# Kernel optimization log

Measured on AMD Instinct MI355X. Metric: run time of the kernel, lower is better.

Reference implementation:

```python
import jax, jax.numpy as jnp
import numpy as np

NG = 64  # number of graphs in the batch (global_add_pool output rows)

def _bn(x, g, b):
    # BatchNorm1d, training-mode batch statistics over dim 0
    mu = x.mean(0)
    var = x.var(0)
    return (x - mu) * jax.lax.rsqrt(var + 1e-5) * g + b

def _ln(x, g, b):
    mu = x.mean(-1, keepdims=True)
    var = x.var(-1, keepdims=True)
    return (x - mu) * jax.lax.rsqrt(var + 1e-5) * g + b

def _gine(x, ei, ea, eps, w1, b1, w2, b2, n):
    # GINEConv: mlp((1+eps)*x + sum_dst ReLU(x[src] + ea))
    msg = jax.nn.relu(x[ei[0]] + ea)
    agg = jax.ops.segment_sum(msg, ei[1], num_segments=n)
    h = (1.0 + eps) * x + agg
    return jax.nn.relu(h @ w1 + b1) @ w2 + b2

def setup_inputs() -> dict:
    key = jax.random.key(0)
    H, L, RW = 128, 4, 16
    Nn, m, kk = 4096, 2, 32
    S = Nn * m; SK = S * kk
    Ei, Eg = 1048576, 65536
    Vatom, Vbond = 128, 16
    ks = jax.random.split(key, 24)
    f = lambda i, shape: jax.random.normal(ks[i], shape, jnp.float32) * 0.02
    # intra edges sampled within each subgraph block to honor locality
    subs = jax.random.randint(ks[11], (Ei,), 0, S)
    src = subs * kk + jax.random.randint(ks[12], (Ei,), 0, kk)
    dst = subs * kk + jax.random.randint(ks[13], (Ei,), 0, kk)
    inp = {
        "atom_emb": f(0, (Vatom, H)), "bond_emb": f(1, (Vbond, H)),
        "rwse_w": f(2, (RW, H)), "rwse_b": jnp.zeros((H,), jnp.float32),
        "rwse": jax.random.uniform(ks[3], (Nn, RW), jnp.float32),
        "l_eps": jnp.zeros((L,), jnp.float32),
        "l_w1": f(4, (L, H, H)), "l_b1": jnp.zeros((L, H), jnp.float32),
        "l_w2": f(5, (L, H, H)), "l_b2": jnp.zeros((L, H), jnp.float32),
        "l_bng": jnp.ones((L, H), jnp.float32), "l_bnb": jnp.zeros((L, H), jnp.float32),
        "g_eps": jnp.zeros((L,), jnp.float32),
        "g_w1": f(6, (L, H, H)), "g_b1": jnp.zeros((L, H), jnp.float32),
        "g_w2": f(7, (L, H, H)), "g_b2": jnp.zeros((L, H), jnp.float32),
        "g_bng": jnp.ones((L, H), jnp.float32), "g_bnb": jnp.zeros((L, H), jnp.float32),
        "bcast_w": f(8, (L, H, H)),
        "cat_w1": f(9, (L, 2 * H, H)), "cat_b1": jnp.zeros((L, H), jnp.float32),
        "cat_w2": f(10, (L, H, H)), "cat_b2": jnp.zeros((L, H), jnp.float32),
        "ln_g": jnp.ones((L, H), jnp.float32), "ln_b": jnp.zeros((L, H), jnp.float32),
        "x_ids": jax.random.randint(ks[14], (SK,), 0, Vatom),
        "intra_ei": jnp.stack([src, dst]),
        "intra_ea_ids": jax.random.randint(ks[15], (Ei,), 0, Vbond),
        "global_ei": jax.random.randint(ks[16], (2, Eg), 0, Nn),
        "global_ea_ids": jax.random.randint(ks[17], (Eg,), 0, Vbond),
        "node_ids": jax.random.randint(ks[18], (SK,), 0, Nn),
        "valid": jax.random.randint(ks[19], (SK,), 0, 2),
        "batch": jnp.sort(jax.random.randint(ks[20], (Nn,), 0, NG)),
        "k": 32,
    }
    return inp

def reference(atom_emb, bond_emb, rwse_w, rwse_b, rwse, l_eps, l_w1, l_b1, l_w2, l_b2, l_bng, l_bnb, g_eps, g_w1, g_b1, g_w2, g_b2, g_bng, g_bnb, bcast_w, cat_w1, cat_b1, cat_w2, cat_b2, ln_g, ln_b, x_ids, intra_ei, intra_ea_ids, global_ei, global_ea_ids, node_ids, valid, batch, k):
    SK = x_ids.shape[0]; Nn = rwse.shape[0]
    S = SK // k; m = S // Nn
    H = atom_emb.shape[1]; L = l_eps.shape[0]
    ea_flat = bond_emb[intra_ea_ids]          # [Ei, H]
    g_ea = bond_emb[global_ea_ids]            # [Eg, H]
    valid_f = valid.astype(jnp.float32)[:, None]
    h = (atom_emb[x_ids] + jax.nn.relu(rwse @ rwse_w + rwse_b)[node_ids]) * valid_f  # [SK, H]
    node_assign = jnp.repeat(jnp.arange(Nn), m)   # [S]
    root_idx = jnp.arange(S) * k                  # subgraph roots in flat layout
    for i in range(L):
        h_in = h
        h_local = _bn(jax.nn.relu(_gine(h, intra_ei, ea_flat, l_eps[i], l_w1[i], l_b1[i], l_w2[i], l_b2[i], SK)), l_bng[i], l_bnb[i])
        # scatter-mean of root reps onto original nodes (each node has exactly m subgraphs)
        h_node = jax.ops.segment_sum(h[root_idx], node_assign, num_segments=Nn) / m
        h_cross = _bn(jax.nn.relu(_gine(h_node, global_ei, g_ea, g_eps[i], g_w1[i], g_b1[i], g_w2[i], g_b2[i], Nn)), g_bng[i], g_bnb[i])
        h_node = h_node + h_cross
        # broadcast projected node reps back to every flat subgraph position
        h_b = jnp.repeat((h_node @ bcast_w[i])[node_assign], k, axis=0)  # [SK, H]
        h_cat = jnp.concatenate([h_local, h_b], axis=-1)
        h_new = _ln(jax.nn.gelu(h_cat @ cat_w1[i] + cat_b1[i], approximate=False) @ cat_w2[i] + cat_b2[i], ln_g[i], ln_b[i])
        h = (h_in + h_new) * valid_f
    # per-subgraph masked mean (h is already zero at invalid rows)
    cnt = valid_f.reshape(S, k, 1).sum(1)
    h_sub = h.reshape(S, k, H).sum(1) / jnp.maximum(cnt, 1.0)   # [S, H]
    h_nodef = h_sub.reshape(Nn, m, H).mean(1)                   # [Nn, H]
    return jax.ops.segment_sum(h_nodef, batch, num_segments=NG) # [NG, H]
```

## Files before the change

kernel.cpp:

```cpp
#include <hip/hip_runtime.h>
#include <hip/hip_bf16.h>

#define H 128
#define HH 16384
#define LNUM 4
#define NN 4096
#define SS 8192
#define SKK 262144
#define EI 1048576
#define EG 65536
#define NGRAPH 64

typedef unsigned short u16;
typedef unsigned int u32;
typedef __attribute__((ext_vector_type(8))) short s16x8;
typedef __attribute__((ext_vector_type(4))) float f32x4;

__device__ __forceinline__ float b2f(u32 u){ return __uint_as_float(u<<16); }
__device__ __forceinline__ u16 f2b(float f){
  union { __hip_bfloat16 b; u16 u; } x;
  x.b=__float2bfloat16(f);
  return x.u;
}
__device__ __forceinline__ void unp8(uint4 v, float* f){
  f[0]=b2f(v.x&0xFFFF); f[1]=b2f(v.x>>16);
  f[2]=b2f(v.y&0xFFFF); f[3]=b2f(v.y>>16);
  f[4]=b2f(v.z&0xFFFF); f[5]=b2f(v.z>>16);
  f[6]=b2f(v.w&0xFFFF); f[7]=b2f(v.w>>16);
}
__device__ __forceinline__ void unp4(uint2 v, float* f){
  f[0]=b2f(v.x&0xFFFF); f[1]=b2f(v.x>>16);
  f[2]=b2f(v.y&0xFFFF); f[3]=b2f(v.y>>16);
}
__device__ __forceinline__ uint4 pk8(const float* f){
  uint4 r;
  r.x=(u32)f2b(f[0])|((u32)f2b(f[1])<<16);
  r.y=(u32)f2b(f[2])|((u32)f2b(f[3])<<16);
  r.z=(u32)f2b(f[4])|((u32)f2b(f[5])<<16);
  r.w=(u32)f2b(f[6])|((u32)f2b(f[7])<<16);
  return r;
}
__device__ __forceinline__ uint2 pk4(const float* f){
  uint2 r;
  r.x=(u32)f2b(f[0])|((u32)f2b(f[1])<<16);
  r.y=(u32)f2b(f[2])|((u32)f2b(f[3])<<16);
  return r;
}

struct CvtArgs {
  const void* p[26];
  int start[27];
};
struct TransArgs { int src[28]; };

__global__ void k_sniff(const u16* __restrict__ a, int* __restrict__ flag){
  __shared__ int cnt;
  if(threadIdx.x==0) cnt=0;
  __syncthreads();
  int big=0;
  for(int i=threadIdx.x;i<2048;i+=256){
    int e=(a[i]>>7)&0xFF;
    if(e>=127) big++;
  }
  atomicAdd(&cnt,big);
  __syncthreads();
  if(threadIdx.x==0) *flag=(cnt<16)?1:0;
}

__global__ void k_convert(CvtArgs args, const int* __restrict__ flag, float* __restrict__ dst){
  int fl=*flag;
  int total=args.start[26];
  for(int i=blockIdx.x*blockDim.x+threadIdx.x;i<total;i+=gridDim.x*blockDim.x){
    int a=0;
    while(args.start[a+1]<=i) a++;
    int j=i-args.start[a];
    float v;
    if(fl) v=b2f(((const u16*)args.p[a])[j]);
    else   v=((const float*)args.p[a])[j];
    dst[i]=v;
  }
}

__global__ __launch_bounds__(256) void k_trans(const float* __restrict__ par, TransArgs ta, u16* __restrict__ wt){
  const float* s=par+ta.src[blockIdx.x];
  u16* d=wt+(size_t)blockIdx.x*HH;
  for(int i=threadIdx.x;i<HH;i+=256){
    int j=i&7, lane=(i>>3)&63, fc=i>>9;
    int n=fc>>2, kc=fc&3, lr=lane&15, lk=lane>>4;
    int outc=n*16+lr, k=kc*32+lk*8+j;
    d[i]=f2b(s[(size_t)k*H+outc]);
  }
}

__global__ void k_cvtbond(const float* __restrict__ b, u16* __restrict__ bb){
  int i=blockIdx.x*blockDim.x+threadIdx.x;
  if(i<16*H) bb[i]=f2b(b[i]);
}

__global__ __launch_bounds__(128) void k_prepw3(const float* __restrict__ w, const float* __restrict__ cb1,
                        const float* __restrict__ stl, const float* __restrict__ gl, const float* __restrict__ bl,
                        u16* __restrict__ wt3p, float* __restrict__ bias3){
  __shared__ float red[128];
  int c=blockIdx.x, k=threadIdx.x;
  float mu=stl[k]*(1.f/262144.f);
  float var=stl[128+k]*(1.f/262144.f)-mu*mu;
  float s=gl[k]*rsqrtf(var+1e-5f);
  float tt=bl[k]-mu*s;
  float wv=w[(size_t)k*H+c];
  int idx=(((c>>4)*4+(k>>5))*64+((k>>3)&3)*16+(c&15))*8+(k&7);
  wt3p[idx]=f2b(s*wv);
  red[k]=tt*wv;
  __syncthreads();
  for(int d=64;d>0;d>>=1){ if(k<d) red[k]+=red[k+d]; __syncthreads(); }
  if(k==0) bias3[c]=cb1[c]+red[0];
}

__global__ void k_hist(const int* __restrict__ idx, int n, int shift, int* __restrict__ cnt){
  for(int i=blockIdx.x*blockDim.x+threadIdx.x;i<n;i+=gridDim.x*blockDim.x)
    atomicAdd(&cnt[idx[i]>>shift],1);
}

__global__ void k_scan(const int* __restrict__ cnt, int* __restrict__ off, int nbins){
  __shared__ int ts[1024];
  int t=threadIdx.x;
  int per=nbins>>10;
  int base=t*per;
  int s=0;
  for(int j=0;j<per;j++) s+=cnt[base+j];
  ts[t]=s;
  __syncthreads();
  for(int d=1;d<1024;d<<=1){
    int v=(t>=d)?ts[t-d]:0;
    __syncthreads();
    ts[t]+=v;
    __syncthreads();
  }
  int ex=(t==0)?0:ts[t-1];
  for(int j=0;j<per;j++){ off[base+j]=ex; ex+=cnt[base+j]; }
}

__global__ void k_scatter_i(const int* __restrict__ ei, const int* __restrict__ ea,
                            const int* __restrict__ off, int* __restrict__ cur, int* __restrict__ pack){
  for(int i=blockIdx.x*blockDim.x+threadIdx.x;i<EI;i+=gridDim.x*blockDim.x){
    int s=ei[i], d=ei[EI+i];
    int sub=d>>5;
    int pos=off[sub]+atomicAdd(&cur[sub],1);
    pack[pos]=((s&31)<<9)|((d&31)<<4)|(ea[i]&15);
  }
}

__global__ __launch_bounds__(128) void k_sortsub(const int* __restrict__ eoff, const int* __restrict__ ecnt,
                                                 int* __restrict__ epack, int* __restrict__ dstoff){
  __shared__ int ein[512];
  __shared__ int eout[512];
  __shared__ int bcnt[32];
  __shared__ int bpos[32];
  int sub=blockIdx.x, t=threadIdx.x;
  int o=eoff[sub];
  int n=ecnt[sub]; if(n>512) n=512;
  for(int i=t;i<n;i+=128) ein[i]=epack[o+i];
  if(t<32) bcnt[t]=0;
  __syncthreads();
  for(int i=t;i<n;i+=128) atomicAdd(&bcnt[(ein[i]>>4)&31],1);
  __syncthreads();
  if(t==0){
    int s=0;
    for(int b=0;b<32;b++){ bpos[b]=s; s+=bcnt[b]; }
  }
  __syncthreads();
  if(t<32) dstoff[sub*32+t]=bpos[t];
  __syncthreads();
  for(int i=t;i<n;i+=128){
    int p=ein[i];
    int pos=atomicAdd(&bpos[(p>>4)&31],1);
    eout[pos]=p;
  }
  __syncthreads();
  for(int i=t;i<n;i+=128) epack[o+i]=eout[i];
}

__global__ void k_scatter_g(const int* __restrict__ ei, const int* __restrict__ ea,
                            const int* __restrict__ off, int* __restrict__ cur, int* __restrict__ pack){
  for(int i=blockIdx.x*blockDim.x+threadIdx.x;i<EG;i+=gridDim.x*blockDim.x){
    int s=ei[i], d=ei[EG+i];
    int pos=off[d]+atomicAdd(&cur[d],1);
    pack[pos]=(s<<4)|(ea[i]&15);
  }
}

__global__ __launch_bounds__(128) void k_rwse(const float* __restrict__ rwse, const float* __restrict__ w,
                      const float* __restrict__ b, float* __restrict__ rf){
  __shared__ float ws[16*128];
  __shared__ float rv[16];
  int n=blockIdx.x, c=threadIdx.x;
  for(int i=c;i<2048;i+=128) ws[i]=w[i];
  if(c<16) rv[c]=rwse[n*16+c];
  __syncthreads();
  float acc=b[c];
  for(int j=0;j<16;j++) acc=fmaf(rv[j],ws[j*128+c],acc);
  rf[(size_t)n*H+c]=fmaxf(acc,0.f);
}

__global__ void k_h0(const float* __restrict__ atom, const float* __restrict__ rf,
                     const int* __restrict__ xids, const int* __restrict__ nids,
                     const int* __restrict__ valid, u16* __restrict__ h){
  int i=blockIdx.x*blockDim.x+threadIdx.x;
  if(i>=SKK*16) return;
  int r=i>>4, q=i&15;
  const float4* ap=(const float4*)(atom+(size_t)xids[r]*H)+q*2;
  const float4* bp=(const float4*)(rf+(size_t)nids[r]*H)+q*2;
  float4 a0=ap[0],a1=ap[1],b0=bp[0],b1=bp[1];
  float vm=valid[r]?1.f:0.f;
  float f[8]={(a0.x+b0.x)*vm,(a0.y+b0.y)*vm,(a0.z+b0.z)*vm,(a0.w+b0.w)*vm,
              (a1.x+b1.x)*vm,(a1.y+b1.y)*vm,(a1.z+b1.z)*vm,(a1.w+b1.w)*vm};
  ((uint4*)h)[i]=pk8(f);
}

__global__ __launch_bounds__(256) void k_fused1(
    const u16* __restrict__ h, const u16* __restrict__ beb,
    const int* __restrict__ eoff, const int* __restrict__ ecnt, const int* __restrict__ epack,
    const int* __restrict__ dstoff,
    const float* __restrict__ epsp, int layer,
    const u16* __restrict__ W1p, const float* __restrict__ b1,
    const u16* __restrict__ W2p, const float* __restrict__ b2,
    u16* __restrict__ Xg, float* __restrict__ stats)
{
  __shared__ u16 hs[64*128];
  __shared__ u16 agx[64*128];
  __shared__ u16 bes[16*128];
  __shared__ int epk[2][512];
  __shared__ int doff[2][32];
  __shared__ int nsh[2];
  __shared__ float sst[256];

  int t=threadIdx.x;
  int grp=t>>7, c=t&127;
  size_t hbase=(size_t)blockIdx.x*64*H;
  {
    const uint4* src=(const uint4*)(h+hbase);
    #pragma unroll
    for(int i0=0;i0<4;i0++){
      int i=t+i0*256;
      u32 row=(u32)(i>>4), colb=(u32)((i&15)*16);
      *(uint4*)((char*)hs+row*256+(colb^((row&7)<<4)))=src[i];
    }
    u32 row=(u32)(t>>4), colb=(u32)((t&15)*16);
    *(uint4*)((char*)bes+row*256+(colb^((row&7)<<4)))=((const uint4*)beb)[t];
    sst[t]=0.f;
  }
  int sub=blockIdx.x*2+grp;
  if(c==0) nsh[grp]=min(ecnt[sub],512);
  if(c<32) doff[grp][c]=dstoff[sub*32+c];
  __syncthreads();
  int n=nsh[grp];
  int o=eoff[sub];
  for(int i=c;i<n;i+=128) epk[grp][i]=epack[o+i];
  __syncthreads();
  int slot=c>>4, chg=c&15;
  u32 cbyte=(u32)chg*16;
  float ep=1.f+epsp[layer];
  #pragma unroll
  for(int k=0;k<4;k++){
    int d=slot*4+k;
    int s0=doff[grp][d];
    int s1=(d==31)?n:doff[grp][d+1];
    float acc[8]={0.f,0.f,0.f,0.f,0.f,0.f,0.f,0.f};
    for(int i=s0;i<s1;i++){
      int p=epk[grp][i];
      u32 srow=(u32)(grp*32+(p>>9));
      u32 erow=(u32)(p&15);
      float hf[8],bf8[8];
      unp8(*(const uint4*)((const char*)hs+srow*256+(cbyte^((srow&7)<<4))),hf);
      unp8(*(const uint4*)((const char*)bes+erow*256+(cbyte^((erow&7)<<4))),bf8);
      #pragma unroll
      for(int j=0;j<8;j++) acc[j]+=fmaxf(hf[j]+bf8[j],0.f);
    }
    u32 drow=(u32)(grp*32+d);
    float hf[8],o8[8];
    unp8(*(const uint4*)((const char*)hs+drow*256+(cbyte^((drow&7)<<4))),hf);
    #pragma unroll
    for(int j=0;j<8;j++) o8[j]=fmaf(ep,hf[j],acc[j]);
    *(uint4*)((char*)agx+drow*256+(cbyte^((drow&7)<<4)))=pk8(o8);
  }
  __syncthreads();
  int wave=t>>6, lane=t&63, lr=lane&15, lk=lane>>4;
  int rl=wave*16+lr;
  u32 rsw=((u32)(rl&7))<<4;
  f32x4 a1[8];
  #pragma unroll
  for(int n8=0;n8<8;n8++) a1[n8]=(f32x4){0.f,0.f,0.f,0.f};
  #pragma unroll
  for(int kc=0;kc<4;kc++){
    u32 cb=(u32)((kc*32+lk*8)*2);
    s16x8 bf=*(const s16x8*)((char*)agx+(u32)rl*256+(cb^rsw));
    #pragma unroll
    for(int n8=0;n8<8;n8++){
      s16x8 af=*(const s16x8*)(W1p+((n8*4+kc)<<9)+lane*8);
      a1[n8]=__builtin_amdgcn_mfma_f32_16x16x32_bf16(af,bf,a1[n8],0,0,0);
    }
  }
  #pragma unroll
  for(int n8=0;n8<8;n8++){
    int c0=n8*16+lk*4;
    float4 b4=*(const float4*)(b1+c0);
    float v[4]={fmaxf(a1[n8][0]+b4.x,0.f),fmaxf(a1[n8][1]+b4.y,0.f),
                fmaxf(a1[n8][2]+b4.z,0.f),fmaxf(a1[n8][3]+b4.w,0.f)};
    *(uint2*)((char*)hs+(u32)rl*256+(((u32)(2*c0))^rsw))=pk4(v);
  }
  f32x4 a2[8];
  #pragma unroll
  for(int n8=0;n8<8;n8++) a2[n8]=(f32x4){0.f,0.f,0.f,0.f};
  #pragma unroll
  for(int kc=0;kc<4;kc++){
    u32 cb=(u32)((kc*32+lk*8)*2);
    s16x8 bf=*(const s16x8*)((char*)hs+(u32)rl*256+(cb^rsw));
    #pragma unroll
    for(int n8=0;n8<8;n8++){
      s16x8 af=*(const s16x8*)(W2p+((n8*4+kc)<<9)+lane*8);
      a2[n8]=__builtin_amdgcn_mfma_f32_16x16x32_bf16(af,bf,a2[n8],0,0,0);
    }
  }
  #pragma unroll
  for(int n8=0;n8<8;n8++){
    int c0=n8*16+lk*4;
    float4 b4=*(const float4*)(b2+c0);
    float v[4]={fmaxf(a2[n8][0]+b4.x,0.f),fmaxf(a2[n8][1]+b4.y,0.f),
                fmaxf(a2[n8][2]+b4.z,0.f),fmaxf(a2[n8][3]+b4.w,0.f)};
    *(uint2*)((char*)agx+(u32)rl*256+(((u32)(2*c0))^rsw))=pk4(v);
    float s[4],q[4];
    #pragma unroll
    for(int j=0;j<4;j++){ s[j]=v[j]; q[j]=v[j]*v[j]; }
    #pragma unroll
    for(int j=0;j<4;j++){
      #pragma unroll
      for(int d=1;d<16;d<<=1){
        s[j]+=__shfl_xor(s[j],d);
        q[j]+=__shfl_xor(q[j],d);
      }
    }
    if(lr==0){
      #pragma unroll
      for(int j=0;j<4;j++){
        atomicAdd(&sst[c0+j],s[j]);
        atomicAdd(&sst[128+c0+j],q[j]);
      }
    }
  }
  __syncthreads();
  uint4* out4=(uint4*)(Xg+hbase);
  #pragma unroll
  for(int p=0;p<4;p++){
    int i=t+p*256;
    u32 row=(u32)(i>>4), colb=(u32)((i&15)*16);
    out4[i]=*(const uint4*)((const char*)agx+row*256+(colb^((row&7)<<4)));
  }
  atomicAdd(&stats[t],sst[t]);
}

__global__ __launch_bounds__(256) void k_mlp2n(
    const u16* __restrict__ A, const u16* __restrict__ W1p, const float* __restrict__ b1,
    const u16* __restrict__ W2p, const float* __restrict__ b2,
    u16* __restrict__ out, float* __restrict__ stats)
{
  __shared__ u16 T[64*128];
  __shared__ float sst[256];
  int t=threadIdx.x;
  sst[t]=0.f;
  int wave=t>>6, lane=t&63, lr=lane&15, lk=lane>>4;
  int rl=wave*16+lr;
  u32 rsw=((u32)(rl&7))<<4;
  int row0=blockIdx.x*64;
  f32x4 a1[8];
  #pragma unroll
  for(int n8=0;n8<8;n8++) a1[n8]=(f32x4){0.f,0.f,0.f,0.f};
  const s16x8* B0=(const s16x8*)(A+(size_t)(row0+rl)*H);
  #pragma unroll
  for(int kc=0;kc<4;kc++){
    s16x8 bf=B0[kc*4+lk];
    #pragma unroll
    for(int n8=0;n8<8;n8++){
      s16x8 af=*(const s16x8*)(W1p+((n8*4+kc)<<9)+lane*8);
      a1[n8]=__builtin_amdgcn_mfma_f32_16x16x32_bf16(af,bf,a1[n8],0,0,0);
    }
  }
  #pragma unroll
  for(int n8=0;n8<8;n8++){
    int c0=n8*16+lk*4;
    float4 b4=*(const float4*)(b1+c0);
    float v[4]={fmaxf(a1[n8][0]+b4.x,0.f),fmaxf(a1[n8][1]+b4.y,0.f),
                fmaxf(a1[n8][2]+b4.z,0.f),fmaxf(a1[n8][3]+b4.w,0.f)};
    *(uint2*)((char*)T+(u32)rl*256+(((u32)(2*c0))^rsw))=pk4(v);
  }
  f32x4 a2[8];
  #pragma unroll
  for(int n8=0;n8<8;n8++) a2[n8]=(f32x4){0.f,0.f,0.f,0.f};
  #pragma unroll
  for(int kc=0;kc<4;kc++){
    u32 cb=(u32)((kc*32+lk*8)*2);
    s16x8 bf=*(const s16x8*)((char*)T+(u32)rl*256+(cb^rsw));
    #pragma unroll
    for(int n8=0;n8<8;n8++){
      s16x8 af=*(const s16x8*)(W2p+((n8*4+kc)<<9)+lane*8);
      a2[n8]=__builtin_amdgcn_mfma_f32_16x16x32_bf16(af,bf,a2[n8],0,0,0);
    }
  }
  #pragma unroll
  for(int n8=0;n8<8;n8++){
    int c0=n8*16+lk*4;
    float4 b4=*(const float4*)(b2+c0);
    float v[4]={fmaxf(a2[n8][0]+b4.x,0.f),fmaxf(a2[n8][1]+b4.y,0.f),
                fmaxf(a2[n8][2]+b4.z,0.f),fmaxf(a2[n8][3]+b4.w,0.f)};
    *(uint2*)((char*)T+(u32)rl*256+(((u32)(2*c0))^rsw))=pk4(v);
    float s[4],q[4];
    #pragma unroll
    for(int j=0;j<4;j++){ s[j]=v[j]; q[j]=v[j]*v[j]; }
    #pragma unroll
    for(int j=0;j<4;j++){
      #pragma unroll
      for(int d=1;d<16;d<<=1){
        s[j]+=__shfl_xor(s[j],d);
        q[j]+=__shfl_xor(q[j],d);
      }
    }
    if(lr==0){
      #pragma unroll
      for(int j=0;j<4;j++){
        atomicAdd(&sst[c0+j],s[j]);
        atomicAdd(&sst[128+c0+j],q[j]);
      }
    }
  }
  __syncthreads();
  uint4* out4=(uint4*)(out+(size_t)row0*H);
  #pragma unroll
  for(int p=0;p<4;p++){
    int i=t+p*256;
    u32 row=(u32)(i>>4), colb=(u32)((i&15)*16);
    out4[i]=*(const uint4*)((const char*)T+row*256+(colb^((row&7)<<4)));
  }
  atomicAdd(&stats[t],sst[t]);
}

__global__ __launch_bounds__(256) void k_bcast(
    const u16* __restrict__ hn, const u16* __restrict__ ag,
    const float* __restrict__ stg, const float* __restrict__ gg, const float* __restrict__ bg,
    const u16* __restrict__ Wbcp, const u16* __restrict__ Wc1p,
    u16* __restrict__ bb)
{
  __shared__ u16 T[64*128];
  __shared__ u16 T2[64*128];
  __shared__ float ssh[128], tsh[128];
  int t=threadIdx.x;
  int row0=blockIdx.x*64;
  if(t<128){
    float mu=stg[t]*(1.f/4096.f);
    float var=stg[128+t]*(1.f/4096.f)-mu*mu;
    float s=gg[t]*rsqrtf(var+1e-5f);
    ssh[t]=s; tsh[t]=bg[t]-mu*s;
  }
  __syncthreads();
  #pragma unroll
  for(int i0=0;i0<4;i0++){
    int i=t+i0*256;
    u32 row=(u32)(i>>4);
    int cb8=(i&15)*8;
    float hv[8],av[8],o8[8];
    unp8(((const uint4*)(hn+(size_t)row0*H))[i],hv);
    unp8(((const uint4*)(ag+(size_t)row0*H))[i],av);
    #pragma unroll
    for(int j=0;j<8;j++) o8[j]=hv[j]+fmaf(av[j],ssh[cb8+j],tsh[cb8+j]);
    *(uint4*)((char*)T+row*256+(((u32)(cb8*2))^((row&7)<<4)))=pk8(o8);
  }
  __syncthreads();
  int wave=t>>6, lane=t&63, lr=lane&15, lk=lane>>4;
  int rl=wave*16+lr;
  u32 rsw=((u32)(rl&7))<<4;
  f32x4 a1[8];
  #pragma unroll
  for(int n8=0;n8<8;n8++) a1[n8]=(f32x4){0.f,0.f,0.f,0.f};
  #pragma unroll
  for(int kc=0;kc<4;kc++){
    u32 cb=(u32)((kc*32+lk*8)*2);
    s16x8 bf=*(const s16x8*)((char*)T+(u32)rl*256+(cb^rsw));
    #pragma unroll
    for(int n8=0;n8<8;n8++){
      s16x8 af=*(const s16x8*)(Wbcp+((n8*4+kc)<<9)+lane*8);
      a1[n8]=__builtin_amdgcn_mfma_f32_16x16x32_bf16(af,bf,a1[n8],0,0,0);
    }
  }
  #pragma unroll
  for(int n8=0;n8<8;n8++){
    int c0=n8*16+lk*4;
    float v[4]={a1[n8][0],a1[n8][1],a1[n8][2],a1[n8][3]};
    *(uint2*)((char*)T2+(u32)rl*256+(((u32)(2*c0))^rsw))=pk4(v);
  }
  f32x4 a2[8];
  #pragma unroll
  for(int n8=0;n8<8;n8++) a2[n8]=(f32x4){0.f,0.f,0.f,0.f};
  #pragma unroll
  for(int kc=0;kc<4;kc++){
    u32 cb=(u32)((kc*32+lk*8)*2);
    s16x8 bf=*(const s16x8*)((char*)T2+(u32)rl*256+(cb^rsw));
    #pragma unroll
    for(int n8=0;n8<8;n8++){
      s16x8 af=*(const s16x8*)(Wc1p+((n8*4+kc)<<9)+lane*8);
      a2[n8]=__builtin_amdgcn_mfma_f32_16x16x32_bf16(af,bf,a2[n8],0,0,0);
    }
  }
  #pragma unroll
  for(int n8=0;n8<8;n8++){
    int c0=n8*16+lk*4;
    float v[4]={a2[n8][0],a2[n8][1],a2[n8][2],a2[n8][3]};
    *(uint2*)((char*)T+(u32)rl*256+(((u32)(2*c0))^rsw))=pk4(v);
  }
  __syncthreads();
  uint4* out4=(uint4*)(bb+(size_t)row0*H);
  #pragma unroll
  for(int p=0;p<4;p++){
    int i=t+p*256;
    u32 row=(u32)(i>>4), colb=(u32)((i&15)*16);
    out4[i]=*(const uint4*)((const char*)T+row*256+(colb^((row&7)<<4)));
  }
}

__global__ __launch_bounds__(256) void k_tail(
    const u16* __restrict__ X, const u16* __restrict__ W3p, const float* __restrict__ bias3,
    const u16* __restrict__ bb,
    const u16* __restrict__ W2p, const float* __restrict__ cb2,
    const float* __restrict__ lng, const float* __restrict__ lnb,
    const int* __restrict__ validv, u16* __restrict__ hio)
{
  __shared__ u16 T[64*128];
  int t=threadIdx.x;
  int wave=t>>6, lane=t&63, lr=lane&15, lk=lane>>4;
  int rl=wave*16+lr;
  u32 rsw=((u32)(rl&7))<<4;
  int row0=blockIdx.x*64;
  f32x4 acc[8];
  #pragma unroll
  for(int n8=0;n8<8;n8++) acc[n8]=(f32x4){0.f,0.f,0.f,0.f};
  const s16x8* B0=(const s16x8*)(X+(size_t)(row0+rl)*H);
  #pragma unroll
  for(int kc=0;kc<4;kc++){
    s16x8 bf=B0[kc*4+lk];
    #pragma unroll
    for(int n8=0;n8<8;n8++){
      s16x8 af=*(const s16x8*)(W3p+((n8*4+kc)<<9)+lane*8);
      acc[n8]=__builtin_amdgcn_mfma_f32_16x16x32_bf16(af,bf,acc[n8],0,0,0);
    }
  }
  #pragma unroll
  for(int n8=0;n8<8;n8++){
    int c0=n8*16+lk*4;
    float4 b4=*(const float4*)(bias3+c0);
    float rb[4];
    unp4(*(const uint2*)(bb+(size_t)blockIdx.x*H+c0),rb);
    float vb[4]={b4.x,b4.y,b4.z,b4.w};
    float v[4];
    #pragma unroll
    for(int j=0;j<4;j++){
      float x=acc[n8][j]+vb[j]+rb[j];
      v[j]=0.5f*x*(1.f+erff(x*0.70710678118654752f));
    }
    *(uint2*)((char*)T+(u32)rl*256+(((u32)(2*c0))^rsw))=pk4(v);
  }
  f32x4 a2[8];
  #pragma unroll
  for(int n8=0;n8<8;n8++) a2[n8]=(f32x4){0.f,0.f,0.f,0.f};
  #pragma unroll
  for(int kc=0;kc<4;kc++){
    u32 cb=(u32)((kc*32+lk*8)*2);
    s16x8 bf=*(const s16x8*)((char*)T+(u32)rl*256+(cb^rsw));
    #pragma unroll
    for(int n8=0;n8<8;n8++){
      s16x8 af=*(const s16x8*)(W2p+((n8*4+kc)<<9)+lane*8);
      a2[n8]=__builtin_amdgcn_mfma_f32_16x16x32_bf16(af,bf,a2[n8],0,0,0);
    }
  }
  {
    float s=0.f,q=0.f;
    #pragma unroll
    for(int n8=0;n8<8;n8++){
      int c0=n8*16+lk*4;
      float4 b4=*(const float4*)(cb2+c0);
      float vb[4]={b4.x,b4.y,b4.z,b4.w};
      #pragma unroll
      for(int j=0;j<4;j++){
        float v=a2[n8][j]+vb[j];
        a2[n8][j]=v;
        s+=v; q+=v*v;
      }
    }
    s+=__shfl_xor(s,16); s+=__shfl_xor(s,32);
    q+=__shfl_xor(q,16); q+=__shfl_xor(q,32);
    float mu=s*(1.f/128.f);
    float rsig=rsqrtf(q*(1.f/128.f)-mu*mu+1e-5f);
    #pragma unroll
    for(int n8=0;n8<8;n8++){
      int c0=n8*16+lk*4;
      float4 g4=*(const float4*)(lng+c0);
      float4 e4=*(const float4*)(lnb+c0);
      float g[4]={g4.x,g4.y,g4.z,g4.w}, e[4]={e4.x,e4.y,e4.z,e4.w};
      float ov[4];
      #pragma unroll
      for(int j=0;j<4;j++) ov[j]=(a2[n8][j]-mu)*rsig*g[j]+e[j];
      *(uint2*)((char*)T+(u32)rl*256+(((u32)(2*c0))^rsw))=pk4(ov);
    }
  }
  __syncthreads();
  uint4* hp=(uint4*)(hio+(size_t)row0*H);
  #pragma unroll
  for(int p=0;p<4;p++){
    int i=t+p*256;
    u32 row=(u32)(i>>4), colb=(u32)((i&15)*16);
    int grow=row0+(int)row;
    uint4 v=*(const uint4*)((const char*)T+row*256+(colb^((row&7)<<4)));
    uint4 r=hp[i];
    float vv[8],rv[8],o8[8];
    unp8(v,vv); unp8(r,rv);
    float vm=validv[grow]?1.f:0.f;
    #pragma unroll
    for(int j=0;j<8;j++) o8[j]=(rv[j]+vv[j])*vm;
    hp[i]=pk8(o8);
  }
}

__global__ void k_npool(const u16* __restrict__ h, u16* __restrict__ hn){
  int i=blockIdx.x*blockDim.x+threadIdx.x;
  if(i>=NN*16) return;
  int n=i>>4, q=i&15;
  const uint4* hp=(const uint4*)h;
  float a[8],b[8],o[8];
  unp8(hp[(size_t)n*1024+q],a);
  unp8(hp[(size_t)n*1024+512+q],b);
  #pragma unroll
  for(int e=0;e<8;e++) o[e]=(a[e]+b[e])*0.5f;
  ((uint4*)hn)[i]=pk8(o);
}

__global__ __launch_bounds__(128) void k_gagg(const u16* __restrict__ hn, const float* __restrict__ be,
                      const int* __restrict__ goff, const int* __restrict__ gcnt,
                      const int* __restrict__ gpack, const float* __restrict__ epsp, int layer,
                      u16* __restrict__ hhg){
  __shared__ float bes[16][128];
  int n=blockIdx.x, c=threadIdx.x;
  for(int i=0;i<16;i++) bes[i][c]=be[i*128+c];
  __syncthreads();
  float acc=0.f;
  int o=goff[n], e=o+gcnt[n];
  for(;o<e;o++){
    int p=gpack[o];
    acc+=fmaxf(b2f(hn[(size_t)(p>>4)*H+c])+bes[p&15][c],0.f);
  }
  hhg[(size_t)n*H+c]=f2b(fmaf(1.f+epsp[layer],b2f(hn[(size_t)n*H+c]),acc));
}

__global__ __launch_bounds__(128) void k_pool(const u16* __restrict__ h, const int* __restrict__ valid,
                      const int* __restrict__ batch, float* __restrict__ oacc){
  __shared__ float cs[2];
  int n=blockIdx.x, c=threadIdx.x;
  if(c<2){
    int s=0;
    for(int j=0;j<32;j++) s+=valid[n*64+c*32+j];
    cs[c]=fmaxf((float)s,1.f);
  }
  __syncthreads();
  size_t base=(size_t)n*64*H;
  float a0=0.f,a1=0.f;
  for(int j=0;j<32;j++){
    a0+=b2f(h[base+(size_t)j*H+c]);
    a1+=b2f(h[base+(size_t)(32+j)*H+c]);
  }
  float nodef=0.5f*(a0/cs[0]+a1/cs[1]);
  atomicAdd(&oacc[batch[n]*H+c],nodef);
}

__global__ void k_out(const float* __restrict__ acc, const int* __restrict__ flag, void* __restrict__ out){
  int i=blockIdx.x*blockDim.x+threadIdx.x;
  if(i>=NGRAPH*H) return;
  if(*flag) ((__hip_bfloat16*)out)[i]=__float2bfloat16(acc[i]);
  else ((float*)out)[i]=acc[i];
}

extern "C" void kernel_launch(void* const* d_in, const int* in_sizes, int n_in,
                              void* d_out, int out_size, void* d_ws, size_t ws_size,
                              hipStream_t stream){
  (void)n_in; (void)out_size;
  int pofs[27]; pofs[0]=0;
  for(int i=0;i<26;i++) pofs[i+1]=pofs[i]+in_sizes[i];
  int ptot=pofs[26];

  char* wsb=(char*)d_ws;
  size_t off=0;
  auto alloc=[&](size_t bytes)->char*{ char* p=wsb+off; off+=(bytes+255)&~(size_t)255; return p; };
  int*   flag =(int*)  alloc(4);
  float* par  =(float*)alloc((size_t)ptot*4);
  u16*   h    =(u16*)  alloc((size_t)SKK*H*2);
  u16*   X    =(u16*)  alloc((size_t)SKK*H*2);
  u16*   wt   =(u16*)  alloc((size_t)28*HH*2);
  u16*   wt3  =(u16*)  alloc((size_t)HH*2);
  float* bias3=(float*)alloc(H*4);
  float* rf   =(float*)alloc((size_t)NN*H*4);
  u16*   bondb=(u16*)  alloc((size_t)16*H*2);
  u16*   hn   =(u16*)  alloc((size_t)NN*H*2);
  u16*   hhg  =(u16*)  alloc((size_t)NN*H*2);
  u16*   ag   =(u16*)  alloc((size_t)NN*H*2);
  u16*   bb   =(u16*)  alloc((size_t)NN*H*2);
  int*   ecnt =(int*)  alloc(SS*4);
  int*   ecur =(int*)  alloc(SS*4);
  int*   gcnt =(int*)  alloc(NN*4);
  int*   gcur =(int*)  alloc(NN*4);
  float* stats=(float*)alloc(LNUM*512*4);
  float* oacc =(float*)alloc((size_t)NGRAPH*H*4);
  size_t zbytes=(size_t)SS*4+SS*4+NN*4+NN*4+LNUM*512*4+(size_t)NGRAPH*H*4;
  int* eoff  =(int*)alloc(SS*4);
  int* epack =(int*)alloc((size_t)EI*4);
  int* dstoff=(int*)alloc((size_t)SS*32*4);
  int* goff  =(int*)alloc(NN*4);
  int* gpack =(int*)alloc((size_t)EG*4);

  if(off>ws_size) return;

  const int* xids =(const int*)d_in[26];
  const int* iei  =(const int*)d_in[27];
  const int* iea  =(const int*)d_in[28];
  const int* gei  =(const int*)d_in[29];
  const int* gea  =(const int*)d_in[30];
  const int* nids =(const int*)d_in[31];
  const int* valid=(const int*)d_in[32];
  const int* batch=(const int*)d_in[33];

  const float* atom=par+pofs[0];
  const float* bond=par+pofs[1];
  const float* rw_w=par+pofs[2];
  const float* rw_b=par+pofs[3];
  const float* rwse=par+pofs[4];
  const float* leps=par+pofs[5];
  const float* lb1 =par+pofs[7];
  const float* lb2 =par+pofs[9];
  const float* lbng=par+pofs[10];
  const float* lbnb=par+pofs[11];
  const float* geps=par+pofs[12];
  const float* gb1 =par+pofs[14];
  const float* gb2 =par+pofs[16];
  const float* gbng=par+pofs[17];
  const float* gbnb=par+pofs[18];
  const float* cw1 =par+pofs[20];
  const float* cb1 =par+pofs[21];
  const float* cb2 =par+pofs[23];
  const float* lngp=par+pofs[24];
  const float* lnbp=par+pofs[25];

  k_sniff<<<1,256,0,stream>>>((const u16*)d_in[0], flag);
  CvtArgs ca;
  for(int i=0;i<26;i++){ ca.p[i]=d_in[i]; ca.start[i]=pofs[i]; }
  ca.start[26]=ptot;
  k_convert<<<1024,256,0,stream>>>(ca, flag, par);

  TransArgs ta;
  for(int l=0;l<LNUM;l++){
    ta.src[l*7+0]=pofs[6]+l*HH;
    ta.src[l*7+1]=pofs[8]+l*HH;
    ta.src[l*7+2]=pofs[13]+l*HH;
    ta.src[l*7+3]=pofs[15]+l*HH;
    ta.src[l*7+4]=pofs[19]+l*HH;
    ta.src[l*7+5]=pofs[20]+l*2*HH+HH;
    ta.src[l*7+6]=pofs[22]+l*HH;
  }
  k_trans<<<28,256,0,stream>>>(par, ta, wt);
  k_cvtbond<<<8,256,0,stream>>>(bond, bondb);

  (void)hipMemsetAsync(ecnt,0,zbytes,stream);

  k_hist<<<2048,256,0,stream>>>(iei+EI, EI, 5, ecnt);
  k_scan<<<1,1024,0,stream>>>(ecnt, eoff, SS);
  k_scatter_i<<<2048,256,0,stream>>>(iei, iea, eoff, ecur, epack);
  k_sortsub<<<SS,128,0,stream>>>(eoff, ecnt, epack, dstoff);
  k_hist<<<512,256,0,stream>>>(gei+EG, EG, 0, gcnt);
  k_scan<<<1,1024,0,stream>>>(gcnt, goff, NN);
  k_scatter_g<<<512,256,0,stream>>>(gei, gea, goff, gcur, gpack);

  k_rwse<<<NN,128,0,stream>>>(rwse, rw_w, rw_b, rf);
  k_h0<<<(SKK*16)/256,256,0,stream>>>(atom, rf, xids, nids, valid, h);

  for(int l=0;l<LNUM;l++){
    float* stl_l=stats+l*512;
    float* stg_l=stats+l*512+256;
    k_fused1<<<SS/2,256,0,stream>>>(h, bondb, eoff, ecnt, epack, dstoff, leps, l,
        wt+(size_t)(l*7+0)*HH, lb1+l*H, wt+(size_t)(l*7+1)*HH, lb2+l*H, X, stl_l);
    k_npool<<<(NN*16)/256,256,0,stream>>>(h, hn);
    k_gagg<<<NN,128,0,stream>>>(hn, bond, goff, gcnt, gpack, geps, l, hhg);
    k_mlp2n<<<NN/64,256,0,stream>>>(hhg, wt+(size_t)(l*7+2)*HH, gb1+l*H,
        wt+(size_t)(l*7+3)*HH, gb2+l*H, ag, stg_l);
    k_bcast<<<NN/64,256,0,stream>>>(hn, ag, stg_l, gbng+l*H, gbnb+l*H,
        wt+(size_t)(l*7+4)*HH, wt+(size_t)(l*7+5)*HH, bb);
    k_prepw3<<<128,128,0,stream>>>(cw1+(size_t)l*2*HH, cb1+l*H, stl_l, lbng+l*H, lbnb+l*H, wt3, bias3);
    k_tail<<<SKK/64,256,0,stream>>>(X, wt3, bias3, bb,
        wt+(size_t)(l*7+6)*HH, cb2+l*H, lngp+l*H, lnbp+l*H, valid, h);
  }
  k_pool<<<NN,128,0,stream>>>(h, valid, batch, oacc);
  k_out<<<(NGRAPH*H+255)/256,256,0,stream>>>(oacc, flag, d_out);
}
```

Baseline: 1.282 ms.

## Fuse previous layer's tail MLP and LayerNorm into next layer's GINE kernel

```diff
diff --git a/kernel.cpp b/kernel.cpp
--- a/kernel.cpp
+++ b/kernel.cpp
@@ -216,6 +216,7 @@
   ((uint4*)h)[i]=pk8(f);
 }
 
+template<int TAIL>
 __global__ __launch_bounds__(256) void k_fused1(
     const u16* __restrict__ h, const u16* __restrict__ beb,
     const int* __restrict__ eoff, const int* __restrict__ ecnt, const int* __restrict__ epack,
@@ -223,20 +224,130 @@
     const float* __restrict__ epsp, int layer,
     const u16* __restrict__ W1p, const float* __restrict__ b1,
     const u16* __restrict__ W2p, const float* __restrict__ b2,
-    u16* __restrict__ Xg, float* __restrict__ stats)
+    u16* __restrict__ Xg, float* __restrict__ stats,
+    const u16* __restrict__ W3p, const float* __restrict__ bias3,
+    const u16* __restrict__ bbv,
+    const u16* __restrict__ Wc2p, const float* __restrict__ cb2,
+    const float* __restrict__ lng, const float* __restrict__ lnb,
+    const int* __restrict__ validv, u16* __restrict__ hio)
 {
   __shared__ u16 hs[64*128];
   __shared__ u16 agx[64*128];
   __shared__ u16 bes[16*128];
   __shared__ int epk[2][512];
   __shared__ int doff[2][32];
-  __shared__ int nsh[2];
   __shared__ float sst[256];
 
   int t=threadIdx.x;
   int grp=t>>7, c=t&127;
   size_t hbase=(size_t)blockIdx.x*64*H;
+  int wave=t>>6, lane=t&63, lr=lane&15, lk=lane>>4;
+  int rl=wave*16+lr;
+  u32 rsw=((u32)(rl&7))<<4;
+  int row0=blockIdx.x*64;
+
   {
+    u32 row=(u32)(t>>4), colb=(u32)((t&15)*16);
+    *(uint4*)((char*)bes+row*256+(colb^((row&7)<<4)))=((const uint4*)beb)[t];
+    sst[t]=0.f;
+  }
+  int sub=blockIdx.x*2+grp;
+  int n=min(ecnt[sub],512);
+  int o=eoff[sub];
+  if(c<32) doff[grp][c]=dstoff[sub*32+c];
+  for(int i=c;i<n;i+=128) epk[grp][i]=epack[o+i];
+
+  if(TAIL){
+    f32x4 a1t[8];
+    #pragma unroll
+    for(int n8=0;n8<8;n8++) a1t[n8]=(f32x4){0.f,0.f,0.f,0.f};
+    const s16x8* B0=(const s16x8*)(Xg+(size_t)(row0+rl)*H);
+    #pragma unroll
+    for(int kc=0;kc<4;kc++){
+      s16x8 bf=B0[kc*4+lk];
+      #pragma unroll
+      for(int n8=0;n8<8;n8++){
+        s16x8 af=*(const s16x8*)(W3p+((n8*4+kc)<<9)+lane*8);
+        a1t[n8]=__builtin_amdgcn_mfma_f32_16x16x32_bf16(af,bf,a1t[n8],0,0,0);
+      }
+    }
+    #pragma unroll
+    for(int n8=0;n8<8;n8++){
+      int c0=n8*16+lk*4;
+      float4 b4=*(const float4*)(bias3+c0);
+      float rb[4];
+      unp4(*(const uint2*)(bbv+(size_t)blockIdx.x*H+c0),rb);
+      float vb[4]={b4.x,b4.y,b4.z,b4.w};
+      float v[4];
+      #pragma unroll
+      for(int j=0;j<4;j++){
+        float x=a1t[n8][j]+vb[j]+rb[j];
+        v[j]=0.5f*x*(1.f+erff(x*0.70710678118654752f));
+      }
+      *(uint2*)((char*)agx+(u32)rl*256+(((u32)(2*c0))^rsw))=pk4(v);
+    }
+    f32x4 a2t[8];
+    #pragma unroll
+    for(int n8=0;n8<8;n8++) a2t[n8]=(f32x4){0.f,0.f,0.f,0.f};
+    #pragma unroll
+    for(int kc=0;kc<4;kc++){
+      u32 cb=(u32)((kc*32+lk*8)*2);
+      s16x8 bf=*(const s16x8*)((char*)agx+(u32)rl*256+(cb^rsw));
+      #pragma unroll
+      for(int n8=0;n8<8;n8++){
+        s16x8 af=*(const s16x8*)(Wc2p+((n8*4+kc)<<9)+lane*8);
+        a2t[n8]=__builtin_amdgcn_mfma_f32_16x16x32_bf16(af,bf,a2t[n8],0,0,0);
+      }
+    }
+    {
+      float s=0.f,q=0.f;
+      #pragma unroll
+      for(int n8=0;n8<8;n8++){
+        int c0=n8*16+lk*4;
+        float4 b4=*(const float4*)(cb2+c0);
+        float vb[4]={b4.x,b4.y,b4.z,b4.w};
+        #pragma unroll
+        for(int j=0;j<4;j++){
+          float v=a2t[n8][j]+vb[j];
+          a2t[n8][j]=v;
+          s+=v; q+=v*v;
+        }
+      }
+      s+=__shfl_xor(s,16); s+=__shfl_xor(s,32);
+      q+=__shfl_xor(q,16); q+=__shfl_xor(q,32);
+      float mu=s*(1.f/128.f);
+      float rsig=rsqrtf(q*(1.f/128.f)-mu*mu+1e-5f);
+      #pragma unroll
+      for(int n8=0;n8<8;n8++){
+        int c0=n8*16+lk*4;
+        float4 g4=*(const float4*)(lng+c0);
+        float4 e4=*(const float4*)(lnb+c0);
+        float g[4]={g4.x,g4.y,g4.z,g4.w}, e[4]={e4.x,e4.y,e4.z,e4.w};
+        float ov[4];
+        #pragma unroll
+        for(int j=0;j<4;j++) ov[j]=(a2t[n8][j]-mu)*rsig*g[j]+e[j];
+        *(uint2*)((char*)agx+(u32)rl*256+(((u32)(2*c0))^rsw))=pk4(ov);
+      }
+    }
+    __syncthreads();
+    uint4* hp=(uint4*)(hio+hbase);
+    #pragma unroll
+    for(int p=0;p<4;p++){
+      int i=t+p*256;
+      u32 row=(u32)(i>>4), colb=(u32)((i&15)*16);
+      int grow=row0+(int)row;
+      uint4 v=*(const uint4*)((const char*)agx+row*256+(colb^((row&7)<<4)));
+      uint4 r=hp[i];
+      float vv[8],rv[8],o8[8];
+      unp8(v,vv); unp8(r,rv);
+      float vm=validv[grow]?1.f:0.f;
+      #pragma unroll
+      for(int j=0;j<8;j++) o8[j]=(rv[j]+vv[j])*vm;
+      uint4 pk=pk8(o8);
+      hp[i]=pk;
+      *(uint4*)((char*)hs+row*256+(colb^((row&7)<<4)))=pk;
+    }
+  } else {
     const uint4* src=(const uint4*)(h+hbase);
     #pragma unroll
     for(int i0=0;i0<4;i0++){
@@ -244,48 +355,52 @@
       u32 row=(u32)(i>>4), colb=(u32)((i&15)*16);
       *(uint4*)((char*)hs+row*256+(colb^((row&7)<<4)))=src[i];
     }
-    u32 row=(u32)(t>>4), colb=(u32)((t&15)*16);
-    *(uint4*)((char*)bes+row*256+(colb^((row&7)<<4)))=((const uint4*)beb)[t];
-    sst[t]=0.f;
-  }
-  int sub=blockIdx.x*2+grp;
-  if(c==0) nsh[grp]=min(ecnt[sub],512);
-  if(c<32) doff[grp][c]=dstoff[sub*32+c];
-  __syncthreads();
-  int n=nsh[grp];
-  int o=eoff[sub];
-  for(int i=c;i<n;i+=128) epk[grp][i]=epack[o+i];
-  __syncthreads();
-  int slot=c>>4, chg=c&15;
-  u32 cbyte=(u32)chg*16;
-  float ep=1.f+epsp[layer];
-  #pragma unroll
-  for(int k=0;k<4;k++){
-    int d=slot*4+k;
-    int s0=doff[grp][d];
-    int s1=(d==31)?n:doff[grp][d+1];
-    float acc[8]={0.f,0.f,0.f,0.f,0.f,0.f,0.f,0.f};
-    for(int i=s0;i<s1;i++){
-      int p=epk[grp][i];
-      u32 srow=(u32)(grp*32+(p>>9));
-      u32 erow=(u32)(p&15);
-      float hf[8],bf8[8];
-      unp8(*(const uint4*)((const char*)hs+srow*256+(cbyte^((srow&7)<<4))),hf);
-      unp8(*(const uint4*)((const char*)bes+erow*256+(cbyte^((erow&7)<<4))),bf8);
-      #pragma unroll
-      for(int j=0;j<8;j++) acc[j]+=fmaxf(hf[j]+bf8[j],0.f);
-    }
-    u32 drow=(u32)(grp*32+d);
-    float hf[8],o8[8];
-    unp8(*(const uint4*)((const char*)hs+drow*256+(cbyte^((drow&7)<<4))),hf);
-    #pragma unroll
-    for(int j=0;j<8;j++) o8[j]=fmaf(ep,hf[j],acc[j]);
-    *(uint4*)((char*)agx+drow*256+(cbyte^((drow&7)<<4)))=pk8(o8);
-  }
-  __syncthreads();
-  int wave=t>>6, lane=t&63, lr=lane&15, lk=lane>>4;
-  int rl=wave*16+lr;
-  u32 rsw=((u32)(rl&7))<<4;
+  }
+  __syncthreads();
+
+  {
+    int slot=c>>4, chg=c&15;
+    u32 cbyte=(u32)chg*16;
+    float ep=1.f+epsp[layer];
+    #pragma unroll
+    for(int k=0;k<4;k++){
+      int d=slot*4+k;
+      int s0=doff[grp][d];
+      int s1=(d==31)?n:doff[grp][d+1];
+      float acc[8]={0.f,0.f,0.f,0.f,0.f,0.f,0.f,0.f};
+      if(s0<s1){
+        int p=epk[grp][s0];
+        u32 srow=(u32)(grp*32+(p>>9));
+        u32 erow=(u32)(p&15);
+        uint4 hv=*(const uint4*)((const char*)hs+srow*256+(cbyte^((srow&7)<<4)));
+        uint4 bv=*(const uint4*)((const char*)bes+erow*256+(cbyte^((erow&7)<<4)));
+        for(int i=s0+1;i<s1;i++){
+          int p2=epk[grp][i];
+          u32 srow2=(u32)(grp*32+(p2>>9));
+          u32 erow2=(u32)(p2&15);
+          uint4 hv2=*(const uint4*)((const char*)hs+srow2*256+(cbyte^((srow2&7)<<4)));
+          uint4 bv2=*(const uint4*)((const char*)bes+erow2*256+(cbyte^((erow2&7)<<4)));
+          float hf[8],bf8[8];
+          unp8(hv,hf); unp8(bv,bf8);
+          #pragma unroll
+          for(int j=0;j<8;j++) acc[j]+=fmaxf(hf[j]+bf8[j],0.f);
+          hv=hv2; bv=bv2;
+        }
+        float hf[8],bf8[8];
+        unp8(hv,hf); unp8(bv,bf8);
+        #pragma unroll
+        for(int j=0;j<8;j++) acc[j]+=fmaxf(hf[j]+bf8[j],0.f);
+      }
+      u32 drow=(u32)(grp*32+d);
+      float hf[8],o8[8];
+      unp8(*(const uint4*)((const char*)hs+drow*256+(cbyte^((drow&7)<<4))),hf);
+      #pragma unroll
+      for(int j=0;j<8;j++) o8[j]=fmaf(ep,hf[j],acc[j]);
+      *(uint4*)((char*)agx+drow*256+(cbyte^((drow&7)<<4)))=pk8(o8);
+    }
+  }
+  __syncthreads();
+
   f32x4 a1[8];
   #pragma unroll
   for(int n8=0;n8<8;n8++) a1[n8]=(f32x4){0.f,0.f,0.f,0.f};
@@ -786,8 +901,17 @@
   for(int l=0;l<LNUM;l++){
     float* stl_l=stats+l*512;
     float* stg_l=stats+l*512+256;
-    k_fused1<<<SS/2,256,0,stream>>>(h, bondb, eoff, ecnt, epack, dstoff, leps, l,
-        wt+(size_t)(l*7+0)*HH, lb1+l*H, wt+(size_t)(l*7+1)*HH, lb2+l*H, X, stl_l);
+    if(l==0){
+      k_fused1<0><<<SS/2,256,0,stream>>>(h, bondb, eoff, ecnt, epack, dstoff, leps, l,
+          wt+(size_t)(l*7+0)*HH, lb1+l*H, wt+(size_t)(l*7+1)*HH, lb2+l*H, X, stl_l,
+          nullptr,nullptr,nullptr,nullptr,nullptr,nullptr,nullptr,nullptr,nullptr);
+    } else {
+      int pl=l-1;
+      k_fused1<1><<<SS/2,256,0,stream>>>(h, bondb, eoff, ecnt, epack, dstoff, leps, l,
+          wt+(size_t)(l*7+0)*HH, lb1+l*H, wt+(size_t)(l*7+1)*HH, lb2+l*H, X, stl_l,
+          wt3, bias3, bb, wt+(size_t)(pl*7+6)*HH, cb2+pl*H,
+          lngp+pl*H, lnbp+pl*H, valid, h);
+    }
     k_npool<<<(NN*16)/256,256,0,stream>>>(h, hn);
     k_gagg<<<NN,128,0,stream>>>(hn, bond, goff, gcnt, gpack, geps, l, hhg);
     k_mlp2n<<<NN/64,256,0,stream>>>(hhg, wt+(size_t)(l*7+2)*HH, gb1+l*H,
@@ -795,6 +919,9 @@
     k_bcast<<<NN/64,256,0,stream>>>(hn, ag, stg_l, gbng+l*H, gbnb+l*H,
         wt+(size_t)(l*7+4)*HH, wt+(size_t)(l*7+5)*HH, bb);
     k_prepw3<<<128,128,0,stream>>>(cw1+(size_t)l*2*HH, cb1+l*H, stl_l, lbng+l*H, lbnb+l*H, wt3, bias3);
+  }
+  {
+    int l=LNUM-1;
     k_tail<<<SKK/64,256,0,stream>>>(X, wt3, bias3, bb,
         wt+(size_t)(l*7+6)*HH, cb2+l*H, lngp+l*H, lnbp+l*H, valid, h);
   }
```

New measurement: 1.219 ms. -4.9%, faster.
